# Performance work log

Hardware: AMD Instinct MI355X
Metric: run time of the kernel (lower is better)

Reference implementation:

```python
import jax, jax.numpy as jnp
import numpy as np
import math

HEAD = 8
D_MODEL = 512
D_K = D_MODEL // HEAD
BS = 1024
HIST = 199


def setup_inputs() -> dict:
    key = jax.random.key(0)
    ks = jax.random.split(key, 9)
    s = 1.0 / math.sqrt(D_MODEL)
    return {
        "current_embed": jax.random.normal(ks[0], (BS, D_MODEL), dtype=jnp.float32),
        "previous_embed": jax.random.normal(ks[1], (BS, HIST, D_MODEL), dtype=jnp.float32),
        "local_attn_mask": jax.random.normal(ks[2], (BS, HIST + 1), dtype=jnp.float32),
        "Wq": jax.random.normal(ks[3], (D_MODEL, D_MODEL), dtype=jnp.float32) * s,
        "bq": jax.random.normal(ks[4], (D_MODEL,), dtype=jnp.float32) * s,
        "Wk": jax.random.normal(ks[5], (D_MODEL, D_MODEL), dtype=jnp.float32) * s,
        "bk": jax.random.normal(ks[6], (D_MODEL,), dtype=jnp.float32) * s,
        "Wv": jax.random.normal(ks[7], (D_MODEL, D_MODEL), dtype=jnp.float32) * s,
        "bv": jax.random.normal(ks[8], (D_MODEL,), dtype=jnp.float32) * s,
    }


def reference(current_embed, previous_embed, local_attn_mask, Wq, bq, Wk, bk, Wv, bv):
    bs = current_embed.shape[0]
    # all_time_embed: [bs, T, d] where T = hist + 1
    all_time = jnp.concatenate([previous_embed, current_embed[:, None, :]], axis=1)
    T = all_time.shape[1]
    # Q: single query per batch -> [bs, head, d_k]
    q = (current_embed @ Wq.T + bq).reshape(bs, HEAD, D_K)
    # K, V over full history -> [bs, T, head, d_k]
    k = (all_time @ Wk.T + bk).reshape(bs, T, HEAD, D_K)
    v = (all_time @ Wv.T + bv).reshape(bs, T, HEAD, D_K)
    # scores: [bs, head, T], scaled; additive mask broadcast over heads
    scores = jnp.einsum("bhd,bthd->bht", q, k) / math.sqrt(D_K)
    norm = jax.nn.softmax(scores + local_attn_mask[:, None, :], axis=-1)
    # weighted sum over time -> [bs, head, d_k] -> [bs, d_model]
    out = jnp.einsum("bht,bthd->bhd", norm, v)
    return out.reshape(bs, D_MODEL)
```

## Files before the change

kernel.cpp:

```cpp
#include <hip/hip_runtime.h>
#include <math.h>

#define DM 512
#define NH 8
#define BS 1024
#define HIST 199
#define TT 200

__device__ __forceinline__ float dot8(const float4& a0, const float4& a1,
                                      const float4& b0, const float4& b1) {
  float p = a0.x * b0.x;
  p = fmaf(a0.y, b0.y, p);
  p = fmaf(a0.z, b0.z, p);
  p = fmaf(a0.w, b0.w, p);
  p = fmaf(a1.x, b1.x, p);
  p = fmaf(a1.y, b1.y, p);
  p = fmaf(a1.z, b1.z, p);
  p = fmaf(a1.w, b1.w, p);
  return p;
}

__device__ __forceinline__ float wred64(float p) {
  p += __shfl_xor(p, 1);
  p += __shfl_xor(p, 2);
  p += __shfl_xor(p, 4);
  p += __shfl_xor(p, 8);
  p += __shfl_xor(p, 16);
  p += __shfl_xor(p, 32);
  return p;
}

__global__ __launch_bounds__(256, 4) void qproj_kernel(
    const float* __restrict__ cur, const float* __restrict__ Wq,
    const float* __restrict__ bq, float* __restrict__ q) {
  const int lane = threadIdx.x & 63;
  const int wave = threadIdx.x >> 6;
  const int b = (blockIdx.x >> 2) * 4 + wave;
  const int j0 = (blockIdx.x & 3) * 128;
  const float* cp = cur + (size_t)b * DM;
  const float4 ca = *(const float4*)(cp + 4 * lane);
  const float4 cb = *(const float4*)(cp + 256 + 4 * lane);
  float keep0 = 0.f, keep1 = 0.f;
  for (int jj = 0; jj < 128; ++jj) {
    const float* wp = Wq + (size_t)(j0 + jj) * DM;
    const float4 wa = *(const float4*)(wp + 4 * lane);
    const float4 wb = *(const float4*)(wp + 256 + 4 * lane);
    float p = wred64(dot8(ca, cb, wa, wb));
    if (jj < 64) {
      if (lane == jj) keep0 = p;
    } else {
      if (lane == (jj - 64)) keep1 = p;
    }
  }
  q[(size_t)b * DM + j0 + lane] = keep0 + bq[j0 + lane];
  q[(size_t)b * DM + j0 + 64 + lane] = keep1 + bq[j0 + 64 + lane];
}

__global__ __launch_bounds__(256, 4) void qk_kernel(
    const float* __restrict__ q, const float* __restrict__ Wk,
    const float* __restrict__ bk, float* __restrict__ qk1,
    float* __restrict__ qc1) {
  __shared__ float q8[8][64];
  const int tid = threadIdx.x;
  const int bg = blockIdx.x >> 3;
  const int h = blockIdx.x & 7;
  for (int i = tid; i < 512; i += 256) {
    const int bl = i >> 6, d = i & 63;
    q8[bl][d] = q[(size_t)(bg * 8 + bl) * DM + h * 64 + d];
  }
  __syncthreads();
  float acc0[8], acc1[8];
#pragma unroll
  for (int bl = 0; bl < 8; ++bl) {
    acc0[bl] = 0.f;
    acc1[bl] = 0.f;
  }
  const int e = tid;
  const float* wkb = Wk + (size_t)h * 64 * DM;
  for (int d4 = 0; d4 < 64; d4 += 4) {
    float w0[4], w1[4];
#pragma unroll
    for (int dd = 0; dd < 4; ++dd) {
      w0[dd] = wkb[(size_t)(d4 + dd) * DM + e];
      w1[dd] = wkb[(size_t)(d4 + dd) * DM + e + 256];
    }
#pragma unroll
    for (int bl = 0; bl < 8; ++bl) {
      const float4 qq = *(const float4*)&q8[bl][d4];
      acc0[bl] = fmaf(qq.x, w0[0], acc0[bl]);
      acc0[bl] = fmaf(qq.y, w0[1], acc0[bl]);
      acc0[bl] = fmaf(qq.z, w0[2], acc0[bl]);
      acc0[bl] = fmaf(qq.w, w0[3], acc0[bl]);
      acc1[bl] = fmaf(qq.x, w1[0], acc1[bl]);
      acc1[bl] = fmaf(qq.y, w1[1], acc1[bl]);
      acc1[bl] = fmaf(qq.z, w1[2], acc1[bl]);
      acc1[bl] = fmaf(qq.w, w1[3], acc1[bl]);
    }
  }
#pragma unroll
  for (int bl = 0; bl < 8; ++bl) {
    const size_t base = ((size_t)(bg * 8 + bl) * NH + h) * DM;
    qk1[base + e] = acc0[bl] * 0.125f;
    qk1[base + e + 256] = acc1[bl] * 0.125f;
  }
  if (tid < 8) {
    float s = 0.f;
    for (int d = 0; d < 64; ++d) s += q8[tid][d] * bk[h * 64 + d];
    qc1[(size_t)(bg * 8 + tid) * NH + h] = s * 0.125f;
  }
}

__global__ __launch_bounds__(512, 4) void attn_kernel(
    const float* __restrict__ cur, const float* __restrict__ prev,
    const float* __restrict__ mask, const float* __restrict__ qk1,
    const float* __restrict__ qc1, const float* __restrict__ Wv,
    const float* __restrict__ bv, float* __restrict__ out) {
  __shared__ float cbuf[2][4][4][DM];
  __shared__ float lbuf[2][4][4];
  const int tid = threadIdx.x;
  const int lane = tid & 63;
  const int wave = tid >> 6;
  const int g = wave & 1;
  const int c = wave >> 1;
  const int b = blockIdx.x;

  float4 ka[4], kb[4];
  float qc[4];
#pragma unroll
  for (int hl = 0; hl < 4; ++hl) {
    const float* kp = qk1 + ((size_t)b * NH + (g * 4 + hl)) * DM;
    ka[hl] = *(const float4*)(kp + 4 * lane);
    kb[hl] = *(const float4*)(kp + 256 + 4 * lane);
    qc[hl] = qc1[(size_t)b * NH + (g * 4 + hl)];
  }
  float4 cA[4], cB[4];
#pragma unroll
  for (int hl = 0; hl < 4; ++hl) {
    cA[hl] = make_float4(0.f, 0.f, 0.f, 0.f);
    cB[hl] = make_float4(0.f, 0.f, 0.f, 0.f);
  }
  float ls0 = 0.f, ls1 = 0.f, ls2 = 0.f, ls3 = 0.f;
  const float* mrow = mask + (size_t)b * TT;
  const int t0 = c * 50;
#pragma unroll 2
  for (int t = t0; t < t0 + 50; ++t) {
    const float* rowp = (t < HIST) ? (prev + ((size_t)b * HIST + t) * DM)
                                   : (cur + (size_t)b * DM);
    const float4 ra = *(const float4*)(rowp + 4 * lane);
    const float4 rb = *(const float4*)(rowp + 256 + 4 * lane);
    float pp[4];
#pragma unroll
    for (int hl = 0; hl < 4; ++hl) pp[hl] = dot8(ra, rb, ka[hl], kb[hl]);
#pragma unroll
    for (int hl = 0; hl < 4; ++hl) pp[hl] = wred64(pp[hl]);
    const float mval = mrow[t];
#pragma unroll
    for (int hl = 0; hl < 4; ++hl) {
      const float w = __expf(pp[hl] + qc[hl] + mval);
      if (hl == 0) ls0 += w;
      if (hl == 1) ls1 += w;
      if (hl == 2) ls2 += w;
      if (hl == 3) ls3 += w;
      cA[hl].x = fmaf(w, ra.x, cA[hl].x);
      cA[hl].y = fmaf(w, ra.y, cA[hl].y);
      cA[hl].z = fmaf(w, ra.z, cA[hl].z);
      cA[hl].w = fmaf(w, ra.w, cA[hl].w);
      cB[hl].x = fmaf(w, rb.x, cB[hl].x);
      cB[hl].y = fmaf(w, rb.y, cB[hl].y);
      cB[hl].z = fmaf(w, rb.z, cB[hl].z);
      cB[hl].w = fmaf(w, rb.w, cB[hl].w);
    }
  }
#pragma unroll
  for (int hl = 0; hl < 4; ++hl) {
    *(float4*)&cbuf[g][c][hl][4 * lane] = cA[hl];
    *(float4*)&cbuf[g][c][hl][256 + 4 * lane] = cB[hl];
  }
  if (lane == 0) {
    lbuf[g][c][0] = ls0;
    lbuf[g][c][1] = ls1;
    lbuf[g][c][2] = ls2;
    lbuf[g][c][3] = ls3;
  }
  __syncthreads();
  const int gh = tid >> 6;
  const int g2 = gh >> 2, h2 = gh & 3;
  const int e0 = (tid & 63) * 8;
  float s0[8];
#pragma unroll
  for (int k = 0; k < 8; ++k) s0[k] = 0.f;
#pragma unroll
  for (int cc = 0; cc < 4; ++cc) {
    const float4 a = *(const float4*)&cbuf[g2][cc][h2][e0];
    const float4 bb = *(const float4*)&cbuf[g2][cc][h2][e0 + 4];
    s0[0] += a.x;
    s0[1] += a.y;
    s0[2] += a.z;
    s0[3] += a.w;
    s0[4] += bb.x;
    s0[5] += bb.y;
    s0[6] += bb.z;
    s0[7] += bb.w;
  }
  const float inv = 1.0f / (lbuf[g2][0][h2] + lbuf[g2][1][h2] +
                            lbuf[g2][2][h2] + lbuf[g2][3][h2]);
  __syncthreads();
  float* cn = &cbuf[0][0][0][0];
  *(float4*)(cn + (size_t)gh * DM + e0) =
      make_float4(s0[0] * inv, s0[1] * inv, s0[2] * inv, s0[3] * inv);
  *(float4*)(cn + (size_t)gh * DM + e0 + 4) =
      make_float4(s0[4] * inv, s0[5] * inv, s0[6] * inv, s0[7] * inv);
  __syncthreads();
  const int hh = wave;
  const float4 na = *(const float4*)(cn + (size_t)hh * DM + 4 * lane);
  const float4 nb = *(const float4*)(cn + (size_t)hh * DM + 256 + 4 * lane);
  float keep = 0.f;
  for (int r = 0; r < 64; ++r) {
    const float* wvp = Wv + (size_t)(hh * 64 + r) * DM;
    const float4 wa = *(const float4*)(wvp + 4 * lane);
    const float4 wb = *(const float4*)(wvp + 256 + 4 * lane);
    float p = wred64(dot8(na, nb, wa, wb));
    if (lane == r) keep = p;
  }
  out[(size_t)b * DM + hh * 64 + lane] = keep + bv[hh * 64 + lane];
}

extern "C" void kernel_launch(void* const* d_in, const int* in_sizes, int n_in,
                              void* d_out, int out_size, void* d_ws,
                              size_t ws_size, hipStream_t stream) {
  const float* cur = (const float*)d_in[0];
  const float* prev = (const float*)d_in[1];
  const float* mask = (const float*)d_in[2];
  const float* Wq = (const float*)d_in[3];
  const float* bq = (const float*)d_in[4];
  const float* Wk = (const float*)d_in[5];
  const float* bk = (const float*)d_in[6];
  const float* Wv = (const float*)d_in[7];
  const float* bv = (const float*)d_in[8];
  float* out = (float*)d_out;

  float* q = (float*)d_ws;
  float* qk1 = q + (size_t)BS * DM;
  float* qc1 = qk1 + (size_t)BS * NH * DM;

  qproj_kernel<<<1024, 256, 0, stream>>>(cur, Wq, bq, q);
  qk_kernel<<<1024, 256, 0, stream>>>(q, Wk, bk, qk1, qc1);
  attn_kernel<<<1024, 512, 0, stream>>>(cur, prev, mask, qk1, qc1, Wv, bv, out);
}
```

Measured before the change: 757.8 us.

## Shrink attn shared memory, prefetch next row, and shuffle-broadcast mask values

The attention kernel's shared buffer shrinks from per-chunk partials to one accumulator per head group, filled by serial read-add-write passes across the four time chunks with a barrier after each. This cuts LDS use, which may allow more resident blocks. The loop now loads the next history row into registers before computing the current one. Mask values are read once per wave and broadcast with shuffles, and the softmax normalisation moves to the output after the Wv projection. The trade-offs are extra barriers and more live registers.

```diff
diff --git a/kernel.cpp b/kernel.cpp
--- a/kernel.cpp
+++ b/kernel.cpp
@@ -115,8 +115,8 @@
     const float* __restrict__ mask, const float* __restrict__ qk1,
     const float* __restrict__ qc1, const float* __restrict__ Wv,
     const float* __restrict__ bv, float* __restrict__ out) {
-  __shared__ float cbuf[2][4][4][DM];
-  __shared__ float lbuf[2][4][4];
+  __shared__ float red[2][4][DM];
+  __shared__ float lred[2][4][4];
   const int tid = threadIdx.x;
   const int lane = tid & 63;
   const int wave = tid >> 6;
@@ -140,20 +140,28 @@
     cB[hl] = make_float4(0.f, 0.f, 0.f, 0.f);
   }
   float ls0 = 0.f, ls1 = 0.f, ls2 = 0.f, ls3 = 0.f;
-  const float* mrow = mask + (size_t)b * TT;
   const int t0 = c * 50;
-#pragma unroll 2
+  const int ml = (lane < 49) ? lane : 49;
+  const float mreg = mask[(size_t)b * TT + t0 + ml];
+
+  const float* rp0 = (t0 < HIST) ? (prev + ((size_t)b * HIST + t0) * DM)
+                                 : (cur + (size_t)b * DM);
+  float4 ra = *(const float4*)(rp0 + 4 * lane);
+  float4 rb = *(const float4*)(rp0 + 256 + 4 * lane);
   for (int t = t0; t < t0 + 50; ++t) {
-    const float* rowp = (t < HIST) ? (prev + ((size_t)b * HIST + t) * DM)
-                                   : (cur + (size_t)b * DM);
-    const float4 ra = *(const float4*)(rowp + 4 * lane);
-    const float4 rb = *(const float4*)(rowp + 256 + 4 * lane);
+    int tn = t + 1;
+    if (tn >= t0 + 50) tn = t0 + 49;
+    const float* np = (tn < HIST) ? (prev + ((size_t)b * HIST + tn) * DM)
+                                  : (cur + (size_t)b * DM);
+    const float4 nra = *(const float4*)(np + 4 * lane);
+    const float4 nrb = *(const float4*)(np + 256 + 4 * lane);
+
     float pp[4];
 #pragma unroll
     for (int hl = 0; hl < 4; ++hl) pp[hl] = dot8(ra, rb, ka[hl], kb[hl]);
 #pragma unroll
     for (int hl = 0; hl < 4; ++hl) pp[hl] = wred64(pp[hl]);
-    const float mval = mrow[t];
+    const float mval = __shfl(mreg, t - t0);
 #pragma unroll
     for (int hl = 0; hl < 4; ++hl) {
       const float w = __expf(pp[hl] + qc[hl] + mval);
@@ -170,50 +178,47 @@
       cB[hl].z = fmaf(w, rb.z, cB[hl].z);
       cB[hl].w = fmaf(w, rb.w, cB[hl].w);
     }
-  }
-#pragma unroll
-  for (int hl = 0; hl < 4; ++hl) {
-    *(float4*)&cbuf[g][c][hl][4 * lane] = cA[hl];
-    *(float4*)&cbuf[g][c][hl][256 + 4 * lane] = cB[hl];
+    ra = nra;
+    rb = nrb;
   }
   if (lane == 0) {
-    lbuf[g][c][0] = ls0;
-    lbuf[g][c][1] = ls1;
-    lbuf[g][c][2] = ls2;
-    lbuf[g][c][3] = ls3;
-  }
-  __syncthreads();
-  const int gh = tid >> 6;
-  const int g2 = gh >> 2, h2 = gh & 3;
-  const int e0 = (tid & 63) * 8;
-  float s0[8];
-#pragma unroll
-  for (int k = 0; k < 8; ++k) s0[k] = 0.f;
-#pragma unroll
+    lred[g][c][0] = ls0;
+    lred[g][c][1] = ls1;
+    lred[g][c][2] = ls2;
+    lred[g][c][3] = ls3;
+  }
   for (int cc = 0; cc < 4; ++cc) {
-    const float4 a = *(const float4*)&cbuf[g2][cc][h2][e0];
-    const float4 bb = *(const float4*)&cbuf[g2][cc][h2][e0 + 4];
-    s0[0] += a.x;
-    s0[1] += a.y;
-    s0[2] += a.z;
-    s0[3] += a.w;
-    s0[4] += bb.x;
-    s0[5] += bb.y;
-    s0[6] += bb.z;
-    s0[7] += bb.w;
-  }
-  const float inv = 1.0f / (lbuf[g2][0][h2] + lbuf[g2][1][h2] +
-                            lbuf[g2][2][h2] + lbuf[g2][3][h2]);
-  __syncthreads();
-  float* cn = &cbuf[0][0][0][0];
-  *(float4*)(cn + (size_t)gh * DM + e0) =
-      make_float4(s0[0] * inv, s0[1] * inv, s0[2] * inv, s0[3] * inv);
-  *(float4*)(cn + (size_t)gh * DM + e0 + 4) =
-      make_float4(s0[4] * inv, s0[5] * inv, s0[6] * inv, s0[7] * inv);
-  __syncthreads();
+    if (c == cc) {
+#pragma unroll
+      for (int hl = 0; hl < 4; ++hl) {
+        float* dst = &red[g][hl][0];
+        if (cc == 0) {
+          *(float4*)(dst + 4 * lane) = cA[hl];
+          *(float4*)(dst + 256 + 4 * lane) = cB[hl];
+        } else {
+          float4 o0 = *(const float4*)(dst + 4 * lane);
+          float4 o1 = *(const float4*)(dst + 256 + 4 * lane);
+          o0.x += cA[hl].x;
+          o0.y += cA[hl].y;
+          o0.z += cA[hl].z;
+          o0.w += cA[hl].w;
+          o1.x += cB[hl].x;
+          o1.y += cB[hl].y;
+          o1.z += cB[hl].z;
+          o1.w += cB[hl].w;
+          *(float4*)(dst + 4 * lane) = o0;
+          *(float4*)(dst + 256 + 4 * lane) = o1;
+        }
+      }
+    }
+    __syncthreads();
+  }
   const int hh = wave;
-  const float4 na = *(const float4*)(cn + (size_t)hh * DM + 4 * lane);
-  const float4 nb = *(const float4*)(cn + (size_t)hh * DM + 256 + 4 * lane);
+  const int g2 = hh >> 2, h2 = hh & 3;
+  const float linv = 1.0f / (lred[g2][0][h2] + lred[g2][1][h2] +
+                             lred[g2][2][h2] + lred[g2][3][h2]);
+  const float4 na = *(const float4*)(&red[g2][h2][0] + 4 * lane);
+  const float4 nb = *(const float4*)(&red[g2][h2][0] + 256 + 4 * lane);
   float keep = 0.f;
   for (int r = 0; r < 64; ++r) {
     const float* wvp = Wv + (size_t)(hh * 64 + r) * DM;
@@ -222,7 +227,7 @@
     float p = wred64(dot8(na, nb, wa, wb));
     if (lane == r) keep = p;
   }
-  out[(size_t)b * DM + hh * 64 + lane] = keep + bv[hh * 64 + lane];
+  out[(size_t)b * DM + hh * 64 + lane] = keep * linv + bv[hh * 64 + lane];
 }
 
 extern "C" void kernel_launch(void* const* d_in, const int* in_sizes, int n_in,
```

Measured after the change: 717.0 us. 1.06x faster.
